# Kernel optimization log

Hardware: AMD Instinct MI355X
Metric: run time of the kernel (lower is better)

## Reference

```python
import jax, jax.numpy as jnp
import numpy as np

N_LEAVES = 8192   # perfect binary tree, depth 13
SEQ = 4096        # sequenceSize
EMB = 100         # embedSize
NCLS = 2          # numClasses


def setup_inputs() -> dict:
    key = jax.random.key(0)
    k = jax.random.split(key, 7)
    return {
        "leaf_seqs": jax.random.normal(k[0], (N_LEAVES, SEQ), dtype=jnp.float32),
        # torch nn.Linear stores weight as [out, in]; y = x @ W.T + b
        "We": jax.random.normal(k[1], (EMB, SEQ), dtype=jnp.float32) / np.sqrt(SEQ).astype(np.float32),
        "be": jax.random.normal(k[2], (EMB,), dtype=jnp.float32) * 0.01,
        "W": jax.random.normal(k[3], (EMB, 2 * EMB), dtype=jnp.float32) / np.sqrt(2 * EMB).astype(np.float32),
        "b": jax.random.normal(k[4], (EMB,), dtype=jnp.float32) * 0.01,
        "Wp": jax.random.normal(k[5], (NCLS, EMB), dtype=jnp.float32) / np.sqrt(EMB).astype(np.float32),
        "bp": jax.random.normal(k[6], (NCLS,), dtype=jnp.float32) * 0.01,
    }


def reference(leaf_seqs, We, be, W, b, Wp, bp):
    # Level-order (tree-batched) evaluation of the recursive RNN over a
    # perfect binary tree. Leaves: relu(embedding(seq)); internal nodes:
    # relu(W @ cat(left, right)); root: projection -> class logits.
    h = jax.nn.relu(leaf_seqs @ We.T + be)              # [n_leaves, emb]
    depth = int(np.log2(N_LEAVES))
    for _ in range(depth):                               # fixed small loop over levels
        # adjacent siblings: reshape gives cat((left, right), dim=1) per pair
        pairs = h.reshape(h.shape[0] // 2, 2 * h.shape[1])  # [n/2, 2*emb]
        h = jax.nn.relu(pairs @ W.T + b)                 # [n/2, emb]
    logits = h @ Wp.T + bp                               # [1, numClasses]
    return logits
```

## Files before the change

### kernel.cpp

```cpp
#include <hip/hip_runtime.h>


typedef _Float16 half_t;
typedef __attribute__((ext_vector_type(8))) _Float16 half8;
typedef __attribute__((ext_vector_type(4))) float floatx4;

__device__ __forceinline__ void gld_lds16(const float* g, float* l) {
  __builtin_amdgcn_global_load_lds((const __attribute__((address_space(1))) void*)g,
                                   (__attribute__((address_space(3))) void*)l, 16, 0, 0);
}

__device__ __forceinline__ void cvt_hilo(const floatx4& a, const floatx4& b, half8& hi, half8& lo) {
#pragma unroll
  for (int j = 0; j < 4; ++j) {
    float v = a[j];
    half_t hh = (half_t)v;
    hi[j] = hh; lo[j] = (half_t)(v - (float)hh);
  }
#pragma unroll
  for (int j = 0; j < 4; ++j) {
    float v = b[j];
    half_t hh = (half_t)v;
    hi[4 + j] = hh; lo[4 + j] = (half_t)(v - (float)hh);
  }
}

__global__ __launch_bounds__(256) void bprep(const float* __restrict__ We,
                                             half_t* __restrict__ Bf) {
  int t = blockIdx.x * 256 + threadIdx.x;
  if (t >= 51200) return;
  int n = t >> 9;
  int kp = t & 511;
  int k0 = kp * 8;
  int ks = k0 >> 5;
  int q = (k0 >> 3) & 3;
  int c = n >> 4, m = n & 15;
  int lane = q * 16 + m;

  const float* src = We + (size_t)n * 4096 + k0;
  half8 hv, lv;
#pragma unroll
  for (int j = 0; j < 8; ++j) {
    float w = src[j];
    half_t hh = (half_t)w;
    hv[j] = hh; lv[j] = (half_t)(w - (float)hh);
  }
  size_t base = (size_t)(ks * 14 + c * 2) * 64 + lane;
  *(half8*)(Bf + base * 8) = hv;
  *(half8*)(Bf + (base + 64) * 8) = lv;
}

__global__ __launch_bounds__(64) void wprep(const float* __restrict__ W,
                                            half_t* __restrict__ Wf) {
  int ks = blockIdx.x / 7, tt = blockIdx.x % 7;
  int lane = threadIdx.x;
  int q = lane >> 4, n = lane & 15;
  int col = tt * 16 + n;
  int kb = ks * 32 + q * 8;
  half8 hv, lv;
#pragma unroll
  for (int j = 0; j < 8; ++j) {
    int k = kb + j;
    float w = (col < 100 && k < 200) ? W[(size_t)col * 200 + k] : 0.f;
    half_t hh = (half_t)w;
    hv[j] = hh; lv[j] = (half_t)(w - (float)hh);
  }
  size_t base = (size_t)(ks * 14 + tt * 2) * 64 + lane;
  *(half8*)(Wf + base * 8) = hv;
  *(half8*)(Wf + (base + 64) * 8) = lv;
}

__global__ __launch_bounds__(512, 1) void leaf_mfma(const float* __restrict__ A,
                                                    const half8* __restrict__ Bf,
                                                    const float* __restrict__ be,
                                                    float* __restrict__ h0) {
  __shared__ __align__(16) float lds[2 * 32 * 260];
  const int tid = threadIdx.x;
  const int lane = tid & 63;
  const int wave = tid >> 6;
  const int q = lane >> 4, m = lane & 15;
  const int r0 = blockIdx.x * 32;

  floatx4 acc[2][7];
#pragma unroll
  for (int t = 0; t < 2; ++t)
#pragma unroll
    for (int c = 0; c < 7; ++c) acc[t][c] = (floatx4){0.f, 0.f, 0.f, 0.f};

  {
    const float* g = A + (size_t)(r0 + wave * 4) * 4096 + lane * 4;
    float* d = lds + (wave * 4) * 260 + lane * 4;
#pragma unroll
    for (int i = 0; i < 4; ++i) gld_lds16(g + (size_t)i * 4096, d + i * 260);
  }
  __syncthreads();

  for (int t = 0; t < 16; ++t) {
    float* cur = lds + (t & 1) * 8320;
    float* nxt = lds + ((t + 1) & 1) * 8320;

    const int ksg = t * 8 + wave;
    const half8* bb = Bf + (size_t)(ksg * 14) * 64 + lane;
    half8 bhi[7], blo[7];
#pragma unroll
    for (int c = 0; c < 7; ++c) { bhi[c] = bb[c * 128]; blo[c] = bb[c * 128 + 64]; }

    if (t < 15) {
      const float* g = A + (size_t)(r0 + wave * 4) * 4096 + (t + 1) * 256 + lane * 4;
      float* d = nxt + (wave * 4) * 260 + lane * 4;
#pragma unroll
      for (int i = 0; i < 4; ++i) gld_lds16(g + (size_t)i * 4096, d + i * 260);
    }

    const float* ap = cur + m * 260 + wave * 32 + q * 8;
    floatx4 a0 = *(const floatx4*)ap;
    floatx4 a1 = *(const floatx4*)(ap + 4);
    floatx4 a2 = *(const floatx4*)(ap + 16 * 260);
    floatx4 a3 = *(const floatx4*)(ap + 16 * 260 + 4);
    half8 ahi[2], alo[2];
    cvt_hilo(a0, a1, ahi[0], alo[0]);
    cvt_hilo(a2, a3, ahi[1], alo[1]);

#pragma unroll
    for (int c = 0; c < 7; ++c) {
      acc[0][c] = __builtin_amdgcn_mfma_f32_16x16x32_f16(ahi[0], bhi[c], acc[0][c], 0, 0, 0);
      acc[1][c] = __builtin_amdgcn_mfma_f32_16x16x32_f16(ahi[1], bhi[c], acc[1][c], 0, 0, 0);
      acc[0][c] = __builtin_amdgcn_mfma_f32_16x16x32_f16(alo[0], bhi[c], acc[0][c], 0, 0, 0);
      acc[1][c] = __builtin_amdgcn_mfma_f32_16x16x32_f16(alo[1], bhi[c], acc[1][c], 0, 0, 0);
      acc[0][c] = __builtin_amdgcn_mfma_f32_16x16x32_f16(ahi[0], blo[c], acc[0][c], 0, 0, 0);
      acc[1][c] = __builtin_amdgcn_mfma_f32_16x16x32_f16(ahi[1], blo[c], acc[1][c], 0, 0, 0);
    }
    __syncthreads();
  }

  float* red = lds;
#pragma unroll
  for (int h = 4; h >= 1; h >>= 1) {
    if (wave >= h && wave < 2 * h) {
      float* d = red + (wave - h) * 3584;
#pragma unroll
      for (int t = 0; t < 2; ++t)
#pragma unroll
        for (int c = 0; c < 7; ++c)
#pragma unroll
          for (int r = 0; r < 4; ++r)
            d[(t * 16 + q * 4 + r) * 112 + c * 16 + m] = acc[t][c][r];
    }
    __syncthreads();
    if (wave < h) {
      const float* s = red + wave * 3584;
#pragma unroll
      for (int t = 0; t < 2; ++t)
#pragma unroll
        for (int c = 0; c < 7; ++c)
#pragma unroll
          for (int r = 0; r < 4; ++r)
            acc[t][c][r] += s[(t * 16 + q * 4 + r) * 112 + c * 16 + m];
    }
    __syncthreads();
  }

  if (wave == 0) {
#pragma unroll
    for (int c = 0; c < 7; ++c) {
      int col = c * 16 + m;
      if (col < 100) {
        float bv = be[col];
#pragma unroll
        for (int t = 0; t < 2; ++t)
#pragma unroll
          for (int r = 0; r < 4; ++r) {
            int row = r0 + t * 16 + q * 4 + r;
            h0[(size_t)row * 100 + col] = fmaxf(acc[t][c][r] + bv, 0.f);
          }
      }
    }
  }
}

template <int NVEC>
__global__ __launch_bounds__(256, 1) void tree_mfma(const float* __restrict__ in,
                                                    float* __restrict__ out,
                                                    const half8* __restrict__ Wf,
                                                    const float* __restrict__ bt) {
  __shared__ __align__(16) float bufA[16 * 228];
  __shared__ __align__(16) float bufB[16 * 228];
  const int tid = threadIdx.x;
  const int lane = tid & 63;
  const int wave = tid >> 6;
  const int q = lane >> 4, m = lane & 15;
  const int t0 = 2 * wave;
  const int t1 = (2 * wave + 1 > 6) ? 6 : 2 * wave + 1;

  half8 wh0[7], wl0[7], wh1[7], wl1[7];
#pragma unroll
  for (int ks = 0; ks < 7; ++ks) {
    wh0[ks] = Wf[(size_t)(ks * 14 + t0 * 2) * 64 + lane];
    wl0[ks] = Wf[(size_t)(ks * 14 + t0 * 2 + 1) * 64 + lane];
    wh1[ks] = Wf[(size_t)(ks * 14 + t1 * 2) * 64 + lane];
    wl1[ks] = Wf[(size_t)(ks * 14 + t1 * 2 + 1) * 64 + lane];
  }
  const int c0 = t0 * 16 + m;
  const int c1 = t1 * 16 + m;
  const float b0 = (c0 < 100) ? bt[c0] : 0.f;
  const float b1 = (c1 < 100) ? bt[c1] : 0.f;

  for (int i = tid; i < 16 * 228; i += 256) { bufA[i] = 0.f; bufB[i] = 0.f; }
  __syncthreads();
  const float* gin = in + (size_t)blockIdx.x * NVEC * 100;
  for (int i = tid; i < NVEC * 100; i += 256) {
    int v = i / 100, j = i - v * 100;
    bufA[(v >> 1) * 228 + (v & 1) * 100 + j] = gin[i];
  }
  __syncthreads();

  float* src = bufA;
  float* dst = bufB;
  constexpr int L = (NVEC == 32) ? 5 : 3;
#pragma unroll
  for (int l = 0; l < L; ++l) {
    const int nout = NVEC >> (l + 1);
    floatx4 acc0 = (floatx4){0.f, 0.f, 0.f, 0.f};
    floatx4 acc1 = (floatx4){0.f, 0.f, 0.f, 0.f};
#pragma unroll
    for (int ks = 0; ks < 7; ++ks) {
      const float* ap = src + m * 228 + ks * 32 + q * 8;
      floatx4 x0 = *(const floatx4*)ap;
      floatx4 x1 = *(const floatx4*)(ap + 4);
      half8 ah, al;
      cvt_hilo(x0, x1, ah, al);
      acc0 = __builtin_amdgcn_mfma_f32_16x16x32_f16(ah, wh0[ks], acc0, 0, 0, 0);
      acc1 = __builtin_amdgcn_mfma_f32_16x16x32_f16(ah, wh1[ks], acc1, 0, 0, 0);
      acc0 = __builtin_amdgcn_mfma_f32_16x16x32_f16(al, wh0[ks], acc0, 0, 0, 0);
      acc1 = __builtin_amdgcn_mfma_f32_16x16x32_f16(al, wh1[ks], acc1, 0, 0, 0);
      acc0 = __builtin_amdgcn_mfma_f32_16x16x32_f16(ah, wl0[ks], acc0, 0, 0, 0);
      acc1 = __builtin_amdgcn_mfma_f32_16x16x32_f16(ah, wl1[ks], acc1, 0, 0, 0);
    }
#pragma unroll
    for (int r = 0; r < 4; ++r) {
      int rowR = q * 4 + r;
      if (rowR < nout) {
        if (c0 < 100)
          dst[(rowR >> 1) * 228 + (rowR & 1) * 100 + c0] = fmaxf(acc0[r] + b0, 0.f);
        if (t1 != t0 && c1 < 100)
          dst[(rowR >> 1) * 228 + (rowR & 1) * 100 + c1] = fmaxf(acc1[r] + b1, 0.f);
      }
    }
    __syncthreads();
    float* tmp = src; src = dst; dst = tmp;
  }
  if (tid < 100) out[(size_t)blockIdx.x * 100 + tid] = src[tid];
}

__global__ __launch_bounds__(128) void proj_kernel(const float* __restrict__ h,
                                                   const float* __restrict__ Wp,
                                                   const float* __restrict__ bp,
                                                   float* __restrict__ out) {
  const int tid = threadIdx.x;
  const int cls = tid >> 6;
  const int l = tid & 63;
  float sum = Wp[cls * 100 + l] * h[l];
  if (l + 64 < 100) sum += Wp[cls * 100 + l + 64] * h[l + 64];
#pragma unroll
  for (int off = 32; off > 0; off >>= 1) sum += __shfl_down(sum, off, 64);
  if (l == 0) out[cls] = sum + bp[cls];
}

extern "C" void kernel_launch(void* const* d_in, const int* in_sizes, int n_in,
                              void* d_out, int out_size, void* d_ws, size_t ws_size,
                              hipStream_t stream) {
  (void)in_sizes; (void)n_in; (void)out_size; (void)ws_size;
  const float* leaf = (const float*)d_in[0];
  const float* We = (const float*)d_in[1];
  const float* be = (const float*)d_in[2];
  const float* W = (const float*)d_in[3];
  const float* b = (const float*)d_in[4];
  const float* Wp = (const float*)d_in[5];
  const float* bp = (const float*)d_in[6];
  float* out = (float*)d_out;

  char* ws = (char*)d_ws;
  half_t* Bf = (half_t*)ws;
  half_t* Wfr = (half_t*)(ws + 1835008);
  float* h0 = (float*)(ws + 1935360);
  float* h1 = (float*)(ws + 5212160);
  float* h2 = (float*)(ws + 5314560);
  float* h3 = (float*)(ws + 5317760);

  bprep<<<dim3(200), dim3(256), 0, stream>>>(We, Bf);
  wprep<<<dim3(49), dim3(64), 0, stream>>>(W, Wfr);
  leaf_mfma<<<dim3(256), dim3(512), 0, stream>>>(leaf, (const half8*)Bf, be, h0);
  tree_mfma<32><<<dim3(256), dim3(256), 0, stream>>>(h0, h1, (const half8*)Wfr, b);
  tree_mfma<32><<<dim3(8), dim3(256), 0, stream>>>(h1, h2, (const half8*)Wfr, b);
  tree_mfma<8><<<dim3(1), dim3(256), 0, stream>>>(h2, h3, (const half8*)Wfr, b);
  proj_kernel<<<dim3(1), dim3(128), 0, stream>>>(h3, Wp, bp, out);
}
```

Before: 256.0 us.

## Triple-buffer leaf input loads with vmcnt waits and fuse projection into last tree kernel

The leaf GEMM kernel moves from double to triple buffering of the LDS A tiles, prefetching two stages ahead. The full __syncthreads is replaced with an explicit vmcnt wait plus s_barrier, so in-flight global-to-LDS loads of the next stage are not drained every iteration. Separately, the final projection is folded into the last tree_mfma launch, which removes one kernel launch. The cost is more LDS use, and correctness now depends on the hand-coded vmcnt encodings matching the number of outstanding loads.

```diff
diff --git a/kernel.cpp b/kernel.cpp
--- a/kernel.cpp
+++ b/kernel.cpp
@@ -4,6 +4,9 @@
 typedef _Float16 half_t;
 typedef __attribute__((ext_vector_type(8))) _Float16 half8;
 typedef __attribute__((ext_vector_type(4))) float floatx4;
+
+#define VMCNT_4 0xF74
+#define VMCNT_0 0xF70
 
 __device__ __forceinline__ void gld_lds16(const float* g, float* l) {
   __builtin_amdgcn_global_load_lds((const __attribute__((address_space(1))) void*)g,
@@ -74,7 +77,7 @@
                                                     const half8* __restrict__ Bf,
                                                     const float* __restrict__ be,
                                                     float* __restrict__ h0) {
-  __shared__ __align__(16) float lds[2 * 32 * 260];
+  __shared__ __align__(16) float lds[3 * 8320];
   const int tid = threadIdx.x;
   const int lane = tid & 63;
   const int wave = tid >> 6;
@@ -87,32 +90,37 @@
 #pragma unroll
     for (int c = 0; c < 7; ++c) acc[t][c] = (floatx4){0.f, 0.f, 0.f, 0.f};
 
+  const float* gbase = A + (size_t)(r0 + wave * 4) * 4096 + lane * 4;
+  const int ldso = (wave * 4) * 260 + lane * 4;
+
   {
-    const float* g = A + (size_t)(r0 + wave * 4) * 4096 + lane * 4;
-    float* d = lds + (wave * 4) * 260 + lane * 4;
-#pragma unroll
-    for (int i = 0; i < 4; ++i) gld_lds16(g + (size_t)i * 4096, d + i * 260);
-  }
-  __syncthreads();
-
+    const float* g0 = gbase;
+    const float* g1 = gbase + 256;
+#pragma unroll
+    for (int i = 0; i < 4; ++i) gld_lds16(g0 + (size_t)i * 4096, lds + ldso + i * 260);
+#pragma unroll
+    for (int i = 0; i < 4; ++i) gld_lds16(g1 + (size_t)i * 4096, lds + 8320 + ldso + i * 260);
+  }
+  __builtin_amdgcn_s_waitcnt(VMCNT_4);
+  __builtin_amdgcn_s_barrier();
+
+  int bc = 0;
   for (int t = 0; t < 16; ++t) {
-    float* cur = lds + (t & 1) * 8320;
-    float* nxt = lds + ((t + 1) & 1) * 8320;
-
     const int ksg = t * 8 + wave;
     const half8* bb = Bf + (size_t)(ksg * 14) * 64 + lane;
     half8 bhi[7], blo[7];
 #pragma unroll
     for (int c = 0; c < 7; ++c) { bhi[c] = bb[c * 128]; blo[c] = bb[c * 128 + 64]; }
 
-    if (t < 15) {
-      const float* g = A + (size_t)(r0 + wave * 4) * 4096 + (t + 1) * 256 + lane * 4;
-      float* d = nxt + (wave * 4) * 260 + lane * 4;
+    if (t < 14) {
+      int bn = bc + 2; if (bn >= 3) bn -= 3;
+      const float* g = gbase + (t + 2) * 256;
+      float* d = lds + bn * 8320 + ldso;
 #pragma unroll
       for (int i = 0; i < 4; ++i) gld_lds16(g + (size_t)i * 4096, d + i * 260);
     }
 
-    const float* ap = cur + m * 260 + wave * 32 + q * 8;
+    const float* ap = lds + bc * 8320 + m * 260 + wave * 32 + q * 8;
     floatx4 a0 = *(const floatx4*)ap;
     floatx4 a1 = *(const floatx4*)(ap + 4);
     floatx4 a2 = *(const floatx4*)(ap + 16 * 260);
@@ -130,7 +138,12 @@
       acc[0][c] = __builtin_amdgcn_mfma_f32_16x16x32_f16(ahi[0], blo[c], acc[0][c], 0, 0, 0);
       acc[1][c] = __builtin_amdgcn_mfma_f32_16x16x32_f16(ahi[1], blo[c], acc[1][c], 0, 0, 0);
     }
-    __syncthreads();
+
+    if (t < 14) __builtin_amdgcn_s_waitcnt(VMCNT_4);
+    else        __builtin_amdgcn_s_waitcnt(VMCNT_0);
+    __builtin_amdgcn_s_barrier();
+
+    bc += 1; if (bc >= 3) bc -= 3;
   }
 
   float* red = lds;
@@ -178,11 +191,13 @@
   }
 }
 
-template <int NVEC>
+template <int NVEC, bool PROJ>
 __global__ __launch_bounds__(256, 1) void tree_mfma(const float* __restrict__ in,
                                                     float* __restrict__ out,
                                                     const half8* __restrict__ Wf,
-                                                    const float* __restrict__ bt) {
+                                                    const float* __restrict__ bt,
+                                                    const float* __restrict__ Wp,
+                                                    const float* __restrict__ bp) {
   __shared__ __align__(16) float bufA[16 * 228];
   __shared__ __align__(16) float bufB[16 * 228];
   const int tid = threadIdx.x;
@@ -249,21 +264,18 @@
     __syncthreads();
     float* tmp = src; src = dst; dst = tmp;
   }
-  if (tid < 100) out[(size_t)blockIdx.x * 100 + tid] = src[tid];
-}
-
-__global__ __launch_bounds__(128) void proj_kernel(const float* __restrict__ h,
-                                                   const float* __restrict__ Wp,
-                                                   const float* __restrict__ bp,
-                                                   float* __restrict__ out) {
-  const int tid = threadIdx.x;
-  const int cls = tid >> 6;
-  const int l = tid & 63;
-  float sum = Wp[cls * 100 + l] * h[l];
-  if (l + 64 < 100) sum += Wp[cls * 100 + l + 64] * h[l + 64];
-#pragma unroll
-  for (int off = 32; off > 0; off >>= 1) sum += __shfl_down(sum, off, 64);
-  if (l == 0) out[cls] = sum + bp[cls];
+  if (PROJ) {
+    if (tid < 128) {
+      int cls = tid >> 6, l = tid & 63;
+      float sum = Wp[cls * 100 + l] * src[l];
+      if (l + 64 < 100) sum += Wp[cls * 100 + l + 64] * src[l + 64];
+#pragma unroll
+      for (int off = 32; off > 0; off >>= 1) sum += __shfl_down(sum, off, 64);
+      if (l == 0) out[cls] = sum + bp[cls];
+    }
+  } else {
+    if (tid < 100) out[(size_t)blockIdx.x * 100 + tid] = src[tid];
+  }
 }
 
 extern "C" void kernel_launch(void* const* d_in, const int* in_sizes, int n_in,
@@ -285,13 +297,11 @@
   float* h0 = (float*)(ws + 1935360);
   float* h1 = (float*)(ws + 5212160);
   float* h2 = (float*)(ws + 5314560);
-  float* h3 = (float*)(ws + 5317760);
 
   bprep<<<dim3(200), dim3(256), 0, stream>>>(We, Bf);
   wprep<<<dim3(49), dim3(64), 0, stream>>>(W, Wfr);
   leaf_mfma<<<dim3(256), dim3(512), 0, stream>>>(leaf, (const half8*)Bf, be, h0);
-  tree_mfma<32><<<dim3(256), dim3(256), 0, stream>>>(h0, h1, (const half8*)Wfr, b);
-  tree_mfma<32><<<dim3(8), dim3(256), 0, stream>>>(h1, h2, (const half8*)Wfr, b);
-  tree_mfma<8><<<dim3(1), dim3(256), 0, stream>>>(h2, h3, (const half8*)Wfr, b);
-  proj_kernel<<<dim3(1), dim3(128), 0, stream>>>(h3, Wp, bp, out);
-}
+  tree_mfma<32, false><<<dim3(256), dim3(256), 0, stream>>>(h0, h1, (const half8*)Wfr, b, nullptr, nullptr);
+  tree_mfma<32, false><<<dim3(8), dim3(256), 0, stream>>>(h1, h2, (const half8*)Wfr, b, nullptr, nullptr);
+  tree_mfma<8, true><<<dim3(1), dim3(256), 0, stream>>>(h2, out, (const half8*)Wfr, b, Wp, bp);
+}
```

Result: faster. 249.8 us (-2.4%).
